# Kernel optimization log

Measured on AMD Instinct MI355X. Metric: run time of the kernel, lower is better.

The kernel has to match this reference:

```python
import jax, jax.numpy as jnp
import numpy as np

HIDDEN = 1024
ATTN = 1024
B, S = 4, 2048


def setup_inputs() -> dict:
    key = jax.random.key(0)
    ks = jax.random.split(key, 6)
    bound = 1.0 / np.sqrt(HIDDEN)
    return {
        "query": jax.random.normal(ks[0], (B, S, HIDDEN), jnp.float32),
        "value": jax.random.normal(ks[1], (B, S, HIDDEN), jnp.float32),
        "Wq": jax.random.uniform(ks[2], (HIDDEN, ATTN), jnp.float32, -bound, bound),
        "bq": jax.random.uniform(ks[3], (ATTN,), jnp.float32, -bound, bound),
        "Wv": jax.random.uniform(ks[4], (HIDDEN, ATTN), jnp.float32, -bound, bound),
        "bv": jax.random.uniform(ks[5], (ATTN,), jnp.float32, -bound, bound),
    }


def reference(query, value, Wq, bq, Wv, bv):
    # Linear projections (torch Linear: x @ W^T + b; here W stored as [in, out])
    q = jnp.einsum("bsh,hd->bsd", query, Wq) + bq  # [B,S,ATTN]
    v = jnp.einsum("bsh,hd->bsd", value, Wv) + bv  # [B,S,ATTN]
    # Unscaled dot-product attention
    scores = jnp.einsum("bqd,bkd->bqk", q, v)       # [B,S,S]
    attn = jax.nn.softmax(scores, axis=-1)
    context = jnp.einsum("bqk,bkd->bqd", attn, v)   # [B,S,ATTN]
    return context
```

## Files before the change

### kernel.cpp

```cpp
#include <hip/hip_runtime.h>
#include <hip/hip_bf16.h>


typedef unsigned short u16;
typedef __attribute__((ext_vector_type(8))) short bf16x8;
typedef __attribute__((ext_vector_type(4))) float f32x4;

typedef __attribute__((address_space(1))) void gvoid_t;
typedef __attribute__((address_space(3))) void svoid_t;

__device__ __forceinline__ void gll16(const void* g, void* l) {
    __builtin_amdgcn_global_load_lds((gvoid_t*)g, (svoid_t*)l, 16, 0, 0);
}

__device__ __forceinline__ u16 bf16rn(float x) {
    unsigned u = __float_as_uint(x);
    unsigned r = (u + 0x7FFFu + ((u >> 16) & 1u)) >> 16;
    return (u16)r;
}
__device__ __forceinline__ float bf2f(u16 h) {
    return __uint_as_float(((unsigned)h) << 16);
}

__device__ __forceinline__ const char* sel3(const char* p0, const char* p1,
                                            const char* p2, int i) {
    return i == 0 ? p0 : (i == 1 ? p1 : p2);
}

#define NSK 48

#define STAGE_A(T, mh) {                                                      \
    const char* _p = sel3(A0z, A1z, A2z, (T) >> 4) + (long)((T) & 15) * 128;  \
    char* _d = smem + (((T) & 1) << 16) + ((mh) << 14) + (w << 10);           \
    gll16(_p + offA##mh##0, _d);                                              \
    gll16(_p + offA##mh##1, _d + 8192); }

#define STAGE_B(T, nh) {                                                      \
    const char* _p = sel3(B0z, B1z, B2z, (T) >> 4) + (long)((T) & 15) * 128;  \
    char* _d = smem + (((T) & 1) << 16) + 32768 + ((nh) << 14) + (w << 10);   \
    gll16(_p + offB##nh##0, _d);                                              \
    gll16(_p + offB##nh##1, _d + 8192); }

#define VM4 { asm volatile("s_waitcnt vmcnt(4)" ::: "memory");                \
              __builtin_amdgcn_sched_barrier(0); }
#define VM0 { asm volatile("s_waitcnt vmcnt(0)" ::: "memory");                \
              __builtin_amdgcn_sched_barrier(0); }

#define PHASE(mh, nh, STAGE, ENDW)                                            \
  {                                                                           \
    if ((nh) == 0) {                                                          \
      _Pragma("unroll") for (int mi = 0; mi < 4; ++mi)                        \
        _Pragma("unroll") for (int ks = 0; ks < 2; ++ks)                      \
          afr[mi][ks] = *(const bf16x8*)(smem + bufb + ((mh) << 14) +         \
              aRdB + mi * 2048 + csw[ks]);                                    \
    }                                                                         \
    bf16x8 bfr[2][2];                                                         \
    _Pragma("unroll") for (int ni = 0; ni < 2; ++ni)                          \
      _Pragma("unroll") for (int ks = 0; ks < 2; ++ks)                        \
        bfr[ni][ks] = *(const bf16x8*)(smem + bufb + ((nh) << 14) +           \
            bRdB + ni * 2048 + csw[ks]);                                      \
    STAGE;                                                                    \
    __builtin_amdgcn_s_barrier();                                             \
    asm volatile("s_waitcnt lgkmcnt(0)" ::: "memory");                        \
    __builtin_amdgcn_sched_barrier(0);                                        \
    __builtin_amdgcn_s_setprio(1);                                            \
    _Pragma("unroll") for (int mi = 0; mi < 4; ++mi)                          \
      _Pragma("unroll") for (int ni = 0; ni < 2; ++ni)                        \
        _Pragma("unroll") for (int ks = 0; ks < 2; ++ks)                      \
          acc[(mh) * 4 + mi][(nh) * 2 + ni] =                                 \
              __builtin_amdgcn_mfma_f32_16x16x32_bf16(                        \
                  afr[mi][ks], bfr[ni][ks],                                   \
                  acc[(mh) * 4 + mi][(nh) * 2 + ni], 0, 0, 0);                \
    __builtin_amdgcn_s_setprio(0);                                            \
    ENDW;                                                                     \
    __builtin_amdgcn_s_barrier();                                             \
  }

template<bool OUTF32>
__global__ __launch_bounds__(512, 2)
void gemm8(const char* a0, const char* a1, const char* a2, long zA,
           const char* b0, const char* b1, const char* b2, long zB,
           float* __restrict__ Of, u16* __restrict__ Ohi, u16* __restrict__ Olo,
           long zC, const float* __restrict__ bias0,
           const float* __restrict__ bias1, int N)
{
    extern __shared__ char smem[];
    const int t = threadIdx.x, lane = t & 63, w = t >> 6;
    const int wm = w >> 2, wn = w & 3;
    const int n0 = blockIdx.x << 8, m0 = blockIdx.y << 8;
    const int z = blockIdx.z;

    const char* A0z = a0 + (long)z * zA;
    const char* A1z = a1 + (long)z * zA;
    const char* A2z = a2 + (long)z * zA;
    const char* B0z = b0 + (long)z * zB;
    const char* B1z = b1 + (long)z * zB;
    const char* B2z = b2 + (long)z * zB;

    const int lr0 = t >> 3;
    const long cg = (long)((((t & 7) ^ ((t >> 3) & 7)) << 4));
    const long offA00 = (long)(m0 + lr0) * 2048 + cg;
    const long offA01 = offA00 + 128L * 2048;
    const long offA10 = (long)(m0 + 64 + lr0) * 2048 + cg;
    const long offA11 = offA10 + 128L * 2048;
    const long offB00 = (long)(n0 + ((lr0 >> 5) << 6) + (lr0 & 31)) * 2048 + cg;
    const long offB01 = offB00 + 128L * 2048;
    const long offB10 = offB00 + 32L * 2048;
    const long offB11 = offB10 + 128L * 2048;

    const int swl = (lane & 7) << 4;
    const int csw[2] = { (((lane >> 4) << 4)) ^ swl,
                         (((lane >> 4) << 4) + 64) ^ swl };
    const int aRdB = (wm * 64 + (lane & 15)) * 128;
    const int bRdB = 32768 + (wn * 32 + (lane & 15)) * 128;

    f32x4 acc[8][4];
#pragma unroll
    for (int i = 0; i < 8; ++i)
#pragma unroll
        for (int j = 0; j < 4; ++j) acc[i][j] = (f32x4)0.f;
    bf16x8 afr[4][2];

    STAGE_A(0, 0); STAGE_B(0, 0); STAGE_A(0, 1); STAGE_B(0, 1);
    STAGE_A(1, 0); STAGE_B(1, 0);
    asm volatile("s_waitcnt vmcnt(4)" ::: "memory");
    __builtin_amdgcn_sched_barrier(0);
    __builtin_amdgcn_s_barrier();

    for (int s = 0; s < NSK - 2; ++s) {
        const int bufb = (s & 1) << 16;
        PHASE(0, 0, STAGE_A(s + 1, 1), );
        PHASE(0, 1, STAGE_B(s + 1, 1), );
        PHASE(1, 0, STAGE_A(s + 2, 0), );
        PHASE(1, 1, STAGE_B(s + 2, 0), VM4);
    }
    {
        const int bufb = ((NSK - 2) & 1) << 16;
        PHASE(0, 0, STAGE_A(NSK - 1, 1), );
        PHASE(0, 1, STAGE_B(NSK - 1, 1), );
        PHASE(1, 0, , );
        PHASE(1, 1, , VM0);
    }
    {
        const int bufb = ((NSK - 1) & 1) << 16;
        PHASE(0, 0, , );
        PHASE(0, 1, , );
        PHASE(1, 0, , );
        PHASE(1, 1, , );
    }

    const int r0 = m0 + wm * 128 + ((lane >> 4) << 2);
    const int c0 = n0 + wn * 64 + (lane & 15);
    if (OUTF32) {
        float* Co = Of + (long)z * zC;
#pragma unroll
        for (int mi = 0; mi < 8; ++mi)
#pragma unroll
            for (int nj = 0; nj < 4; ++nj)
#pragma unroll
                for (int r = 0; r < 4; ++r)
                    Co[(long)(r0 + mi * 16 + r) * N + c0 + nj * 16] =
                        acc[mi][nj][r];
    } else {
        const float* bs = z ? bias1 : bias0;
        float bc[4];
#pragma unroll
        for (int nj = 0; nj < 4; ++nj) bc[nj] = bs[c0 + nj * 16];
        u16* Oh = Ohi + (long)z * zC;
        u16* Ol = Olo + (long)z * zC;
#pragma unroll
        for (int mi = 0; mi < 8; ++mi)
#pragma unroll
            for (int nj = 0; nj < 4; ++nj)
#pragma unroll
                for (int r = 0; r < 4; ++r) {
                    float x = acc[mi][nj][r] + bc[nj];
                    long o = (long)(r0 + mi * 16 + r) * N + c0 + nj * 16;
                    u16 h = bf16rn(x);
                    Oh[o] = h;
                    Ol[o] = bf16rn(x - bf2f(h));
                }
    }
}

__global__ __launch_bounds__(256)
void gemm_pv(const u16* __restrict__ Ah, const u16* __restrict__ Bh,
             const u16* __restrict__ Bl, float* __restrict__ Of,
             int N, int K, long sA, long sB, long sC)
{
    __shared__ __align__(16) u16 sm[12288];
    u16* Ash = sm;
    u16* Bsh = sm + 4096;
    u16* Bsl = sm + 8192;

    const long zb = blockIdx.z;
    Ah += zb * sA; Bh += zb * sB; Bl += zb * sB;

    const int t = threadIdx.x, lane = t & 63, wv = t >> 6;
    const int wr = wv >> 1, wc = wv & 1;
    const int m0 = blockIdx.y << 7, n0 = blockIdx.x << 7;

    const int srow = (wv << 1) * 16 + (lane >> 2);
    const int scol = (lane & 3) << 4;

    const char* pAh0 = (const char*)(Ah + (long)(m0 + srow) * K) + scol;
    const char* pAh1 = pAh0 + (long)16 * K * 2;
    const char* pBh0 = (const char*)(Bh + (long)(n0 + srow) * K) + scol;
    const char* pBh1 = pBh0 + (long)16 * K * 2;
    const char* pBl0 = (const char*)(Bl + (long)(n0 + srow) * K) + scol;
    const char* pBl1 = pBl0 + (long)16 * K * 2;

    u16* lAh0 = Ash + wv * 1024; u16* lAh1 = lAh0 + 512;
    u16* lBh0 = Bsh + wv * 1024; u16* lBh1 = lBh0 + 512;
    u16* lBl0 = Bsl + wv * 1024; u16* lBl1 = lBl0 + 512;

    const int afo = (wr * 64 + (lane & 15)) * 32 + (lane >> 4) * 8;
    const int bfo = (wc * 64 + (lane & 15)) * 32 + (lane >> 4) * 8;

    f32x4 acc[4][4];
#pragma unroll
    for (int i = 0; i < 4; ++i)
#pragma unroll
        for (int j = 0; j < 4; ++j) acc[i][j] = (f32x4)0.f;

    for (int k0 = 0; k0 < K; k0 += 32) {
        gll16(pAh0, lAh0); gll16(pAh1, lAh1);
        gll16(pBh0, lBh0); gll16(pBh1, lBh1);
        gll16(pBl0, lBl0); gll16(pBl1, lBl1);
        pAh0 += 64; pAh1 += 64; pBh0 += 64; pBh1 += 64; pBl0 += 64; pBl1 += 64;
        __syncthreads();

        bf16x8 ah[4], bh[4], bl[4];
#pragma unroll
        for (int i = 0; i < 4; ++i) {
            ah[i] = *(const bf16x8*)(Ash + afo + i * 512);
            bh[i] = *(const bf16x8*)(Bsh + bfo + i * 512);
            bl[i] = *(const bf16x8*)(Bsl + bfo + i * 512);
        }
#pragma unroll
        for (int i = 0; i < 4; ++i)
#pragma unroll
            for (int j = 0; j < 4; ++j)
                acc[i][j] = __builtin_amdgcn_mfma_f32_16x16x32_bf16(ah[i], bh[j], acc[i][j], 0, 0, 0);
#pragma unroll
        for (int i = 0; i < 4; ++i)
#pragma unroll
            for (int j = 0; j < 4; ++j)
                acc[i][j] = __builtin_amdgcn_mfma_f32_16x16x32_bf16(ah[i], bl[j], acc[i][j], 0, 0, 0);
        __syncthreads();
    }

#pragma unroll
    for (int i = 0; i < 4; ++i)
#pragma unroll
        for (int j = 0; j < 4; ++j) {
            const int col = n0 + wc * 64 + j * 16 + (lane & 15);
            const int row0 = m0 + wr * 64 + i * 16 + ((lane >> 4) << 2);
#pragma unroll
            for (int r = 0; r < 4; ++r)
                Of[zb * sC + (long)(row0 + r) * N + col] = acc[i][j][r];
        }
}

__global__ __launch_bounds__(256)
void split_f32(const float* __restrict__ in, u16* __restrict__ hi, u16* __restrict__ lo)
{
    long i = ((long)blockIdx.x * 256 + threadIdx.x) * 4;
    float4 v = *(const float4*)(in + i);
    ushort4 h, l;
    h.x = bf16rn(v.x); l.x = bf16rn(v.x - bf2f(h.x));
    h.y = bf16rn(v.y); l.y = bf16rn(v.y - bf2f(h.y));
    h.z = bf16rn(v.z); l.z = bf16rn(v.z - bf2f(h.z));
    h.w = bf16rn(v.w); l.w = bf16rn(v.w - bf2f(h.w));
    *(ushort4*)(hi + i) = h;
    *(ushort4*)(lo + i) = l;
}

__global__ __launch_bounds__(256)
void tsplit_w(const float* __restrict__ W, u16* __restrict__ hi, u16* __restrict__ lo)
{
    __shared__ float tile[32][33];
    const int n0v = blockIdx.x * 32, k0 = blockIdx.y * 32;
    const int r = threadIdx.x >> 5, c = threadIdx.x & 31;
#pragma unroll
    for (int it = 0; it < 4; ++it)
        tile[r + it * 8][c] = W[(long)(k0 + r + it * 8) * 1024 + n0v + c];
    __syncthreads();
#pragma unroll
    for (int it = 0; it < 4; ++it) {
        const int rr = r + it * 8;
        float x = tile[c][rr];
        u16 h = bf16rn(x);
        long o = (long)(n0v + rr) * 1024 + k0 + c;
        hi[o] = h;
        lo[o] = bf16rn(x - bf2f(h));
    }
}

__global__ __launch_bounds__(256)
void tr_bf16(const u16* __restrict__ src, u16* __restrict__ dst)
{
    __shared__ u16 tile[32][33];
    src += (long)blockIdx.z * 2048 * 1024;
    dst += (long)blockIdx.z * 1024 * 2048;
    const int s0 = blockIdx.x * 32, d0 = blockIdx.y * 32;
    const int r = threadIdx.x >> 5, c = threadIdx.x & 31;
#pragma unroll
    for (int it = 0; it < 4; ++it)
        tile[r + it * 8][c] = src[(long)(s0 + r + it * 8) * 1024 + d0 + c];
    __syncthreads();
#pragma unroll
    for (int it = 0; it < 4; ++it) {
        const int rr = r + it * 8;
        dst[(long)(d0 + rr) * 2048 + s0 + c] = tile[c][rr];
    }
}

__global__ __launch_bounds__(256)
void softmax_p(const float* __restrict__ S, u16* __restrict__ P)
{
    const float* p = S + (long)blockIdx.x * 2048;
    u16* o = P + (long)blockIdx.x * 2048;
    const int t = threadIdx.x;

    float4 x0 = *(const float4*)&p[t * 4];
    float4 x1 = *(const float4*)&p[1024 + t * 4];

    float mx = fmaxf(fmaxf(fmaxf(x0.x, x0.y), fmaxf(x0.z, x0.w)),
                     fmaxf(fmaxf(x1.x, x1.y), fmaxf(x1.z, x1.w)));
#pragma unroll
    for (int off = 32; off; off >>= 1) mx = fmaxf(mx, __shfl_xor(mx, off));

    __shared__ float red[8];
    if ((t & 63) == 0) red[t >> 6] = mx;
    __syncthreads();
    mx = fmaxf(fmaxf(red[0], red[1]), fmaxf(red[2], red[3]));

    x0.x = __expf(x0.x - mx); x0.y = __expf(x0.y - mx);
    x0.z = __expf(x0.z - mx); x0.w = __expf(x0.w - mx);
    x1.x = __expf(x1.x - mx); x1.y = __expf(x1.y - mx);
    x1.z = __expf(x1.z - mx); x1.w = __expf(x1.w - mx);

    float sm2 = (x0.x + x0.y + x0.z + x0.w) + (x1.x + x1.y + x1.z + x1.w);
#pragma unroll
    for (int off = 32; off; off >>= 1) sm2 += __shfl_xor(sm2, off);
    if ((t & 63) == 0) red[4 + (t >> 6)] = sm2;
    __syncthreads();
    sm2 = (red[4] + red[5]) + (red[6] + red[7]);

    const float inv = 1.0f / sm2;
    ushort4 y;
    y.x = bf16rn(x0.x * inv); y.y = bf16rn(x0.y * inv);
    y.z = bf16rn(x0.z * inv); y.w = bf16rn(x0.w * inv);
    *(ushort4*)(o + t * 4) = y;
    y.x = bf16rn(x1.x * inv); y.y = bf16rn(x1.y * inv);
    y.z = bf16rn(x1.z * inv); y.w = bf16rn(x1.w * inv);
    *(ushort4*)(o + 1024 + t * 4) = y;
}

extern "C" void kernel_launch(void* const* d_in, const int* in_sizes, int n_in,
                              void* d_out, int out_size, void* d_ws, size_t ws_size,
                              hipStream_t stream)
{
    const float* query = (const float*)d_in[0];
    const float* value = (const float*)d_in[1];
    const float* Wq    = (const float*)d_in[2];
    const float* bq    = (const float*)d_in[3];
    const float* Wv    = (const float*)d_in[4];
    const float* bv    = (const float*)d_in[5];
    float* out = (float*)d_out;

    char* W = (char*)d_ws;
    u16* qx_hi = (u16*)(W);
    u16* qx_lo = qx_hi + 8388608;
    u16* vx_hi = qx_lo + 8388608;
    u16* vx_lo = vx_hi + 8388608;
    float* sc  = (float*)W;
    u16* q_hi  = (u16*)(W + 67108864);
    u16* q_lo  = q_hi + 8388608;
    u16* p     = (u16*)(W + 67108864);
    u16* v_hi  = (u16*)(W + 100663296);
    u16* v_lo  = v_hi + 8388608;
    u16* vT_hi = (u16*)(W + 134217728);
    u16* vT_lo = vT_hi + 8388608;
    u16* WqT_hi = (u16*)(W + 167772160);
    u16* WqT_lo = WqT_hi + 1048576;
    u16* WvT_hi = WqT_lo + 1048576;
    u16* WvT_lo = WvT_hi + 1048576;

    hipFuncSetAttribute((const void*)&gemm8<false>,
                        hipFuncAttributeMaxDynamicSharedMemorySize, 131072);
    hipFuncSetAttribute((const void*)&gemm8<true>,
                        hipFuncAttributeMaxDynamicSharedMemorySize, 131072);

    split_f32<<<8192, 256, 0, stream>>>(query, qx_hi, qx_lo);
    split_f32<<<8192, 256, 0, stream>>>(value, vx_hi, vx_lo);
    tsplit_w<<<dim3(32, 32), 256, 0, stream>>>(Wq, WqT_hi, WqT_lo);
    tsplit_w<<<dim3(32, 32), 256, 0, stream>>>(Wv, WvT_hi, WvT_lo);

    gemm8<false><<<dim3(4, 32, 2), 512, 131072, stream>>>(
        (const char*)qx_hi, (const char*)qx_hi, (const char*)qx_lo, 33554432L,
        (const char*)WqT_hi, (const char*)WqT_lo, (const char*)WqT_hi, 4194304L,
        nullptr, q_hi, q_lo, 16777216L, bq, bv, 1024);

    tr_bf16<<<dim3(64, 32, 4), 256, 0, stream>>>(v_hi, vT_hi);
    tr_bf16<<<dim3(64, 32, 4), 256, 0, stream>>>(v_lo, vT_lo);

    gemm8<true><<<dim3(8, 8, 4), 512, 131072, stream>>>(
        (const char*)q_hi, (const char*)q_hi, (const char*)q_lo, 4194304L,
        (const char*)v_hi, (const char*)v_lo, (const char*)v_hi, 4194304L,
        sc, nullptr, nullptr, 4194304L, nullptr, nullptr, 2048);

    softmax_p<<<8192, 256, 0, stream>>>(sc, p);

    gemm_pv<<<dim3(8, 16, 4), 256, 0, stream>>>(
        p, vT_hi, vT_lo, out,
        1024, 2048, 2048L * 2048, 1024L * 2048, 2048L * 1024);
}
```

Before: 441.7 us.

## Add pipelined 256x128 PV GEMM, XCD-aware block mapping, and fused vectorized transpose

Replaces the simple 128x128 single-buffered PV GEMM with a 512-thread, double-buffered, swizzled-LDS kernel that streams the hi and lo V planes as one concatenated K dimension. The two projection/score GEMMs now use a 1D grid remapped so blocks sharing a batch or row panel land on the same XCD, aiming at better L2 reuse. The two bf16 transposes become a single launch with 64x64 tiles and short4 accesses. The cost is more complex code, hardcoded shapes and larger shared memory per block.

```diff
diff --git a/kernel.cpp b/kernel.cpp
--- a/kernel.cpp
+++ b/kernel.cpp
@@ -76,7 +76,7 @@
     __builtin_amdgcn_s_barrier();                                             \
   }
 
-template<bool OUTF32>
+template<bool OUTF32, int SCHEME>
 __global__ __launch_bounds__(512, 2)
 void gemm8(const char* a0, const char* a1, const char* a2, long zA,
            const char* b0, const char* b1, const char* b2, long zB,
@@ -87,8 +87,19 @@
     extern __shared__ char smem[];
     const int t = threadIdx.x, lane = t & 63, w = t >> 6;
     const int wm = w >> 2, wn = w & 3;
-    const int n0 = blockIdx.x << 8, m0 = blockIdx.y << 8;
-    const int z = blockIdx.z;
+
+    const int bid = blockIdx.x;
+    const int xcd = bid & 7, bi = bid >> 3;
+    int m0, n0, z;
+    if (SCHEME == 0) {
+        z = xcd >> 1;
+        m0 = (((xcd & 1) << 2) | (bi >> 3)) << 8;
+        n0 = (bi & 7) << 8;
+    } else {
+        m0 = ((xcd << 2) | (bi >> 3)) << 8;
+        n0 = (bi & 3) << 8;
+        z = (bi >> 2) & 1;
+    }
 
     const char* A0z = a0 + (long)z * zA;
     const char* A1z = a1 + (long)z * zA;
@@ -183,83 +194,128 @@
     }
 }
 
-__global__ __launch_bounds__(256)
-void gemm_pv(const u16* __restrict__ Ah, const u16* __restrict__ Bh,
-             const u16* __restrict__ Bl, float* __restrict__ Of,
-             int N, int K, long sA, long sB, long sC)
-{
-    __shared__ __align__(16) u16 sm[12288];
-    u16* Ash = sm;
-    u16* Bsh = sm + 4096;
-    u16* Bsl = sm + 8192;
-
-    const long zb = blockIdx.z;
-    Ah += zb * sA; Bh += zb * sB; Bl += zb * sB;
-
-    const int t = threadIdx.x, lane = t & 63, wv = t >> 6;
-    const int wr = wv >> 1, wc = wv & 1;
-    const int m0 = blockIdx.y << 7, n0 = blockIdx.x << 7;
-
-    const int srow = (wv << 1) * 16 + (lane >> 2);
-    const int scol = (lane & 3) << 4;
-
-    const char* pAh0 = (const char*)(Ah + (long)(m0 + srow) * K) + scol;
-    const char* pAh1 = pAh0 + (long)16 * K * 2;
-    const char* pBh0 = (const char*)(Bh + (long)(n0 + srow) * K) + scol;
-    const char* pBh1 = pBh0 + (long)16 * K * 2;
-    const char* pBl0 = (const char*)(Bl + (long)(n0 + srow) * K) + scol;
-    const char* pBl1 = pBl0 + (long)16 * K * 2;
-
-    u16* lAh0 = Ash + wv * 1024; u16* lAh1 = lAh0 + 512;
-    u16* lBh0 = Bsh + wv * 1024; u16* lBh1 = lBh0 + 512;
-    u16* lBl0 = Bsl + wv * 1024; u16* lBl1 = lBl0 + 512;
-
-    const int afo = (wr * 64 + (lane & 15)) * 32 + (lane >> 4) * 8;
-    const int bfo = (wc * 64 + (lane & 15)) * 32 + (lane >> 4) * 8;
-
-    f32x4 acc[4][4];
-#pragma unroll
-    for (int i = 0; i < 4; ++i)
-#pragma unroll
-        for (int j = 0; j < 4; ++j) acc[i][j] = (f32x4)0.f;
-
-    for (int k0 = 0; k0 < K; k0 += 32) {
-        gll16(pAh0, lAh0); gll16(pAh1, lAh1);
-        gll16(pBh0, lBh0); gll16(pBh1, lBh1);
-        gll16(pBl0, lBl0); gll16(pBl1, lBl1);
-        pAh0 += 64; pAh1 += 64; pBh0 += 64; pBh1 += 64; pBl0 += 64; pBl1 += 64;
-        __syncthreads();
-
-        bf16x8 ah[4], bh[4], bl[4];
-#pragma unroll
-        for (int i = 0; i < 4; ++i) {
-            ah[i] = *(const bf16x8*)(Ash + afo + i * 512);
-            bh[i] = *(const bf16x8*)(Bsh + bfo + i * 512);
-            bl[i] = *(const bf16x8*)(Bsl + bfo + i * 512);
-        }
-#pragma unroll
-        for (int i = 0; i < 4; ++i)
-#pragma unroll
-            for (int j = 0; j < 4; ++j)
-                acc[i][j] = __builtin_amdgcn_mfma_f32_16x16x32_bf16(ah[i], bh[j], acc[i][j], 0, 0, 0);
-#pragma unroll
-        for (int i = 0; i < 4; ++i)
-#pragma unroll
-            for (int j = 0; j < 4; ++j)
-                acc[i][j] = __builtin_amdgcn_mfma_f32_16x16x32_bf16(ah[i], bl[j], acc[i][j], 0, 0, 0);
-        __syncthreads();
-    }
-
-#pragma unroll
-    for (int i = 0; i < 4; ++i)
-#pragma unroll
-        for (int j = 0; j < 4; ++j) {
-            const int col = n0 + wc * 64 + j * 16 + (lane & 15);
-            const int row0 = m0 + wr * 64 + i * 16 + ((lane >> 4) << 2);
-#pragma unroll
-            for (int r = 0; r < 4; ++r)
-                Of[zb * sC + (long)(row0 + r) * N + col] = acc[i][j][r];
-        }
+#define PVNSK 64
+
+#define PV_STAGE_A(T, mh) {                                                   \
+    const char* _p = Ap + (long)((T) & 31) * 128;                             \
+    char* _d = smem + (((T) & 1) * 49152) + ((mh) << 14) + (w << 10);         \
+    gll16(_p + offA##mh##0, _d);                                              \
+    gll16(_p + offA##mh##1, _d + 8192); }
+
+#define PV_STAGE_B(T, nh) {                                                   \
+    const char* _p = (((T) >> 5) ? Bl : Bh) + (long)((T) & 31) * 128;         \
+    char* _d = smem + (((T) & 1) * 49152) + 32768 + ((nh) << 13) + (w << 10); \
+    gll16(_p + offB##nh, _d); }
+
+#define PVM3 { asm volatile("s_waitcnt vmcnt(3)" ::: "memory");               \
+               __builtin_amdgcn_sched_barrier(0); }
+
+#define PVPHASE(mh, nh, STAGE, ENDW)                                          \
+  {                                                                           \
+    if ((nh) == 0) {                                                          \
+      _Pragma("unroll") for (int mi = 0; mi < 4; ++mi)                        \
+        _Pragma("unroll") for (int ks = 0; ks < 2; ++ks)                      \
+          afr[mi][ks] = *(const bf16x8*)(smem + bufb + ((mh) << 14) +         \
+              aRdB + mi * 2048 + csw[ks]);                                    \
+    }                                                                         \
+    bf16x8 bfr[2];                                                            \
+    _Pragma("unroll") for (int ks = 0; ks < 2; ++ks)                          \
+      bfr[ks] = *(const bf16x8*)(smem + bufb + 32768 + ((nh) << 13) +         \
+          bRdB + csw[ks]);                                                    \
+    STAGE;                                                                    \
+    __builtin_amdgcn_s_barrier();                                             \
+    asm volatile("s_waitcnt lgkmcnt(0)" ::: "memory");                        \
+    __builtin_amdgcn_sched_barrier(0);                                        \
+    __builtin_amdgcn_s_setprio(1);                                            \
+    _Pragma("unroll") for (int mi = 0; mi < 4; ++mi)                          \
+      _Pragma("unroll") for (int ks = 0; ks < 2; ++ks)                        \
+        acc[(mh) * 4 + mi][nh] =                                              \
+            __builtin_amdgcn_mfma_f32_16x16x32_bf16(                          \
+                afr[mi][ks], bfr[ks], acc[(mh) * 4 + mi][nh], 0, 0, 0);       \
+    __builtin_amdgcn_s_setprio(0);                                            \
+    ENDW;                                                                     \
+    __builtin_amdgcn_s_barrier();                                             \
+  }
+
+__global__ __launch_bounds__(512, 2)
+void gemm8pv(const char* pA, const char* vTh, const char* vTl,
+             float* __restrict__ Of)
+{
+    extern __shared__ char smem[];
+    const int t = threadIdx.x, lane = t & 63, w = t >> 6;
+    const int wm = w >> 2, wn = w & 3;
+
+    const int bid = blockIdx.x;
+    const int xcd = bid & 7, bi = bid >> 3;
+    const int z  = xcd >> 1;
+    const int m0 = ((((xcd & 1) << 2) | (bi >> 3)) << 8);
+    const int n0 = (bi & 7) << 7;
+
+    const char* Ap = pA  + (long)z * 8388608;
+    const char* Bh = vTh + (long)z * 4194304;
+    const char* Bl = vTl + (long)z * 4194304;
+
+    const int lr0 = t >> 3;
+    const long cg = (long)((((t & 7) ^ ((t >> 3) & 7)) << 4));
+    const long offA00 = (long)(m0 + lr0) * 4096 + cg;
+    const long offA01 = offA00 + 64L * 4096;
+    const long offA10 = (long)(m0 + 128 + lr0) * 4096 + cg;
+    const long offA11 = offA10 + 64L * 4096;
+    const long offB0  = (long)(n0 + lr0) * 4096 + cg;
+    const long offB1  = (long)(n0 + 64 + lr0) * 4096 + cg;
+
+    const int swl = (lane & 7) << 4;
+    const int csw[2] = { (((lane >> 4) << 4)) ^ swl,
+                         (((lane >> 4) << 4) + 64) ^ swl };
+    const int aRdB = (wm * 64 + (lane & 15)) * 128;
+    const int bRdB = (wn * 16 + (lane & 15)) * 128;
+
+    f32x4 acc[8][2];
+#pragma unroll
+    for (int i = 0; i < 8; ++i) { acc[i][0] = (f32x4)0.f; acc[i][1] = (f32x4)0.f; }
+    bf16x8 afr[4][2];
+
+    PV_STAGE_A(0, 0); PV_STAGE_B(0, 0); PV_STAGE_A(0, 1); PV_STAGE_B(0, 1);
+    PV_STAGE_A(1, 0); PV_STAGE_B(1, 0);
+    asm volatile("s_waitcnt vmcnt(3)" ::: "memory");
+    __builtin_amdgcn_sched_barrier(0);
+    __builtin_amdgcn_s_barrier();
+
+    for (int s = 0; s < PVNSK - 2; ++s) {
+        const int bufb = (s & 1) * 49152;
+        PVPHASE(0, 0, PV_STAGE_A(s + 1, 1), );
+        PVPHASE(0, 1, PV_STAGE_B(s + 1, 1), );
+        PVPHASE(1, 0, PV_STAGE_A(s + 2, 0), );
+        PVPHASE(1, 1, PV_STAGE_B(s + 2, 0), PVM3);
+    }
+    {
+        const int bufb = ((PVNSK - 2) & 1) * 49152;
+        PVPHASE(0, 0, PV_STAGE_A(PVNSK - 1, 1), );
+        PVPHASE(0, 1, PV_STAGE_B(PVNSK - 1, 1), );
+        PVPHASE(1, 0, , );
+        PVPHASE(1, 1, , VM0);
+    }
+    {
+        const int bufb = ((PVNSK - 1) & 1) * 49152;
+        PVPHASE(0, 0, , );
+        PVPHASE(0, 1, , );
+        PVPHASE(1, 0, , );
+        PVPHASE(1, 1, , );
+    }
+
+    float* Co = Of + (long)z * 2097152;
+    const int r0 = m0 + wm * 64 + ((lane >> 4) << 2);
+    const int c0 = n0 + wn * 16 + (lane & 15);
+#pragma unroll
+    for (int mh = 0; mh < 2; ++mh)
+#pragma unroll
+        for (int mi = 0; mi < 4; ++mi)
+#pragma unroll
+            for (int nh = 0; nh < 2; ++nh)
+#pragma unroll
+                for (int r = 0; r < 4; ++r)
+                    Co[(long)(r0 + mh * 128 + mi * 16 + r) * 1024 +
+                       c0 + nh * 64] = acc[mh * 4 + mi][nh][r];
 }
 
 __global__ __launch_bounds__(256)
@@ -298,21 +354,30 @@
 }
 
 __global__ __launch_bounds__(256)
-void tr_bf16(const u16* __restrict__ src, u16* __restrict__ dst)
-{
-    __shared__ u16 tile[32][33];
-    src += (long)blockIdx.z * 2048 * 1024;
-    dst += (long)blockIdx.z * 1024 * 2048;
-    const int s0 = blockIdx.x * 32, d0 = blockIdx.y * 32;
-    const int r = threadIdx.x >> 5, c = threadIdx.x & 31;
-#pragma unroll
-    for (int it = 0; it < 4; ++it)
-        tile[r + it * 8][c] = src[(long)(s0 + r + it * 8) * 1024 + d0 + c];
+void tr2_bf16(const u16* __restrict__ v_hi, const u16* __restrict__ v_lo,
+              u16* __restrict__ vT_hi, u16* __restrict__ vT_lo)
+{
+    __shared__ u16 tile[64][68];
+    const int pl = blockIdx.z & 1, b = blockIdx.z >> 1;
+    const u16* src = (pl ? v_lo : v_hi) + (long)b * 2097152;
+    u16* dst = (pl ? vT_lo : vT_hi) + (long)b * 2097152;
+    const int s0 = blockIdx.x * 64, d0 = blockIdx.y * 64;
+    const int t = threadIdx.x;
+    const int rr = t >> 4, c4 = (t & 15) * 4;
+#pragma unroll
+    for (int it = 0; it < 4; ++it) {
+        const int s = it * 16 + rr;
+        *(short4*)&tile[s][c4] =
+            *(const short4*)(src + (long)(s0 + s) * 1024 + d0 + c4);
+    }
     __syncthreads();
 #pragma unroll
     for (int it = 0; it < 4; ++it) {
-        const int rr = r + it * 8;
-        dst[(long)(d0 + rr) * 2048 + s0 + c] = tile[c][rr];
+        const int d = it * 16 + rr;
+        short4 o;
+        o.x = tile[c4 + 0][d]; o.y = tile[c4 + 1][d];
+        o.z = tile[c4 + 2][d]; o.w = tile[c4 + 3][d];
+        *(short4*)(dst + (long)(d0 + d) * 2048 + s0 + c4) = o;
     }
 }
 
@@ -388,32 +453,32 @@
     u16* WvT_hi = WqT_lo + 1048576;
     u16* WvT_lo = WvT_hi + 1048576;
 
-    hipFuncSetAttribute((const void*)&gemm8<false>,
+    hipFuncSetAttribute((const void*)&gemm8<false, 1>,
                         hipFuncAttributeMaxDynamicSharedMemorySize, 131072);
-    hipFuncSetAttribute((const void*)&gemm8<true>,
+    hipFuncSetAttribute((const void*)&gemm8<true, 0>,
                         hipFuncAttributeMaxDynamicSharedMemorySize, 131072);
+    hipFuncSetAttribute((const void*)&gemm8pv,
+                        hipFuncAttributeMaxDynamicSharedMemorySize, 98304);
 
     split_f32<<<8192, 256, 0, stream>>>(query, qx_hi, qx_lo);
     split_f32<<<8192, 256, 0, stream>>>(value, vx_hi, vx_lo);
     tsplit_w<<<dim3(32, 32), 256, 0, stream>>>(Wq, WqT_hi, WqT_lo);
     tsplit_w<<<dim3(32, 32), 256, 0, stream>>>(Wv, WvT_hi, WvT_lo);
 
-    gemm8<false><<<dim3(4, 32, 2), 512, 131072, stream>>>(
+    gemm8<false, 1><<<256, 512, 131072, stream>>>(
         (const char*)qx_hi, (const char*)qx_hi, (const char*)qx_lo, 33554432L,
         (const char*)WqT_hi, (const char*)WqT_lo, (const char*)WqT_hi, 4194304L,
         nullptr, q_hi, q_lo, 16777216L, bq, bv, 1024);
 
-    tr_bf16<<<dim3(64, 32, 4), 256, 0, stream>>>(v_hi, vT_hi);
-    tr_bf16<<<dim3(64, 32, 4), 256, 0, stream>>>(v_lo, vT_lo);
-
-    gemm8<true><<<dim3(8, 8, 4), 512, 131072, stream>>>(
+    tr2_bf16<<<dim3(32, 16, 8), 256, 0, stream>>>(v_hi, v_lo, vT_hi, vT_lo);
+
+    gemm8<true, 0><<<256, 512, 131072, stream>>>(
         (const char*)q_hi, (const char*)q_hi, (const char*)q_lo, 4194304L,
         (const char*)v_hi, (const char*)v_lo, (const char*)v_hi, 4194304L,
         sc, nullptr, nullptr, 4194304L, nullptr, nullptr, 2048);
 
     softmax_p<<<8192, 256, 0, stream>>>(sc, p);
 
-    gemm_pv<<<dim3(8, 16, 4), 256, 0, stream>>>(
-        p, vT_hi, vT_lo, out,
-        1024, 2048, 2048L * 2048, 1024L * 2048, 2048L * 1024);
-}
+    gemm8pv<<<256, 512, 98304, stream>>>(
+        (const char*)p, (const char*)vT_hi, (const char*)vT_lo, out);
+}
```

New measurement: 416.6 us. 5.7% less time.
